# Optimization experiments

Measured on AMD Instinct MI355X. Metric: run time of the kernel, lower is better.

The kernel has to match this reference:

```python
import jax, jax.numpy as jnp
import numpy as np

N = 50000      # nodes
E = 800000     # edges
IN = 128       # in_dim
OUT = 64       # out_dim
NEG_SLOPE = 0.01  # F.leaky_relu default


def setup_inputs() -> dict:
    key = jax.random.key(0)
    k1, k2, k3, k4, k5 = jax.random.split(key, 5)
    h = jax.random.normal(k1, (N, IN), dtype=jnp.float32)
    # xavier-normal-ish scale for the two linear layers
    W_fc = jax.random.normal(k2, (OUT, IN), dtype=jnp.float32) * (2.0 / (IN + OUT)) ** 0.5
    W_attn = jax.random.normal(k3, (2 * OUT,), dtype=jnp.float32) * (2.0 / (2 * OUT + 1)) ** 0.5
    src = jax.random.randint(k4, (E,), 0, N)
    dst = jax.random.randint(k5, (E,), 0, N)
    return {"h": h, "W_fc": W_fc, "W_attn": W_attn, "src": src, "dst": dst}


def reference(h, W_fc, W_attn, src, dst):
    # z = fc(h): [N, OUT]
    z = jnp.einsum("ni,oi->no", h, W_fc)
    d = z.shape[-1]
    # per-edge attention logit: attn_fc(cat([z_src, z_dst])) == z_src@a_l + z_dst@a_r
    a_l, a_r = W_attn[:d], W_attn[d:]
    zs = z[src]                                   # [E, OUT] gather
    e = jax.nn.leaky_relu(zs @ a_l + z[dst] @ a_r, negative_slope=NEG_SLOPE)  # [E]
    # segment softmax over incoming edges of each dst node
    m = jax.ops.segment_max(e, dst, num_segments=N)          # [N]
    ex = jnp.exp(e - m[dst])                                  # [E]
    denom = jax.ops.segment_sum(ex, dst, num_segments=N)      # [N]
    alpha = ex / denom[dst]                                    # [E]
    # weighted scatter-sum of source features
    out = jax.ops.segment_sum(alpha[:, None] * zs, dst, num_segments=N)  # [N, OUT]
    return out
```

## Files before the change

### kernel.cpp

```cpp
#include <hip/hip_runtime.h>
#include <hip/hip_bf16.h>
#include <math.h>

#define IN_DIM 128
#define OUT_DIM 64
#define NEG_SLOPE 0.01f
#define BCAP 1536
#define EPT 32

typedef __attribute__((ext_vector_type(8))) short bf8_t;
typedef __attribute__((ext_vector_type(4))) float f4_t;

__device__ __forceinline__ bf8_t pack8(float4 a, float4 b) {
    union { bf8_t v; __hip_bfloat162 h[4]; } u;
    u.h[0] = __float22bfloat162_rn(make_float2(a.x, a.y));
    u.h[1] = __float22bfloat162_rn(make_float2(a.z, a.w));
    u.h[2] = __float22bfloat162_rn(make_float2(b.x, b.y));
    u.h[3] = __float22bfloat162_rn(make_float2(b.z, b.w));
    return u.v;
}

__global__ __launch_bounds__(256) void k_front(
    const int* __restrict__ src, const int* __restrict__ dst,
    int* __restrict__ bucket_cursor, unsigned* __restrict__ tmp, int E,
    const float4* __restrict__ h4, const float4* __restrict__ W4,
    const float* __restrict__ Wattn,
    __hip_bfloat16* __restrict__ zb, float* __restrict__ s_l, float* __restrict__ s_r,
    int N, int NP1)
{
    __shared__ int cntA[1024];
    __shared__ int gbase[1024];

    const int t = threadIdx.x;

    if (blockIdx.x < NP1) {
        const int base_e = blockIdx.x * (256 * EPT);

        for (int b = t; b < 1024; b += 256) cntA[b] = 0;
        __syncthreads();

        unsigned pArr[EPT];
        unsigned short rArr[EPT];
        #pragma unroll
        for (int i = 0; i < EPT; i++) {
            int ei = base_e + i * 256 + t;
            if (ei < E) {
                int s = src[ei], d = dst[ei];
                int b = d >> 6;
                pArr[i] = ((unsigned)b << 22) | ((unsigned)s << 6) | (unsigned)(d & 63);
                rArr[i] = (unsigned short)atomicAdd(&cntA[b], 1);
            } else {
                pArr[i] = 0xFFFFFFFFu;
            }
        }
        __syncthreads();

        for (int b = t; b < 1024; b += 256)
            if (cntA[b] > 0)
                gbase[b] = atomicAdd(&bucket_cursor[b], cntA[b]);
        __syncthreads();

        #pragma unroll
        for (int i = 0; i < EPT; i++) {
            unsigned p = pArr[i];
            if (p == 0xFFFFFFFFu) continue;
            int b = p >> 22;
            int slot = gbase[b] + rArr[i];
            if (slot < BCAP)
                tmp[(size_t)b * BCAP + slot] = p;
        }
    } else {
        const int lane = t & 63;
        const int wv   = t >> 6;
        const int col  = lane & 15, quad = lane >> 4;
        const int n0   = (blockIdx.x - NP1) * 64 + wv * 16;
        if (n0 >= N) return;

        bf8_t bf[4][4];
        #pragma unroll
        for (int ns = 0; ns < 4; ns++) {
            const float4* wrow = W4 + (size_t)(ns * 16 + col) * (IN_DIM / 4);
            #pragma unroll
            for (int kb = 0; kb < 4; kb++) {
                float4 x = wrow[kb * 8 + quad * 2];
                float4 y = wrow[kb * 8 + quad * 2 + 1];
                bf[kb][ns] = pack8(x, y);
            }
        }

        const int  na = n0 + col;
        const bool nv = (na < N);
        const float4* hrow = h4 + (size_t)(nv ? na : 0) * (IN_DIM / 4);
        const float4 zero = make_float4(0.f, 0.f, 0.f, 0.f);

        f4_t acc[4];
        #pragma unroll
        for (int ns = 0; ns < 4; ns++) acc[ns] = (f4_t){0.f, 0.f, 0.f, 0.f};

        #pragma unroll
        for (int kb = 0; kb < 4; kb++) {
            float4 x = nv ? hrow[kb * 8 + quad * 2]     : zero;
            float4 y = nv ? hrow[kb * 8 + quad * 2 + 1] : zero;
            bf8_t a = pack8(x, y);
            #pragma unroll
            for (int ns = 0; ns < 4; ns++)
                acc[ns] = __builtin_amdgcn_mfma_f32_16x16x32_bf16(a, bf[kb][ns], acc[ns], 0, 0, 0);
        }

        float alv[4], arv[4];
        #pragma unroll
        for (int ns = 0; ns < 4; ns++) {
            alv[ns] = Wattn[ns * 16 + col];
            arv[ns] = Wattn[OUT_DIM + ns * 16 + col];
        }
        #pragma unroll
        for (int r = 0; r < 4; r++) {
            const int nn = n0 + quad * 4 + r;
            float pl = acc[0][r] * alv[0] + acc[1][r] * alv[1] + acc[2][r] * alv[2] + acc[3][r] * alv[3];
            float pr = acc[0][r] * arv[0] + acc[1][r] * arv[1] + acc[2][r] * arv[2] + acc[3][r] * arv[3];
            #pragma unroll
            for (int o = 1; o < 16; o <<= 1) {
                pl += __shfl_xor(pl, o, 64);
                pr += __shfl_xor(pr, o, 64);
            }
            if (nn < N) {
                __hip_bfloat16* zr = zb + (size_t)nn * OUT_DIM;
                #pragma unroll
                for (int ns = 0; ns < 4; ns++)
                    zr[ns * 16 + col] = __float2bfloat16(acc[ns][r]);
                if (col == 0) { s_l[nn] = pl; s_r[nn] = pr; }
            }
        }
    }
}

__global__ __launch_bounds__(256) void k_tail(
    const unsigned* __restrict__ tmp, const int* __restrict__ bucket_cnt,
    const float* __restrict__ s_l, const float* __restrict__ s_r,
    const uint4* __restrict__ zb4, float4* __restrict__ out4, int N)
{
    __shared__ uint2 se[BCAP];
    __shared__ unsigned p2s[BCAP];
    __shared__ float exs[BCAP];
    __shared__ int cnt_s[64], off_s[64];
    __shared__ float srs[64];

    const int b = blockIdx.x, t = threadIdx.x;
    const int lane = t & 63;
    const int nbase = b * 64;
    int mb = bucket_cnt[b];
    if (mb > BCAP) mb = BCAP;

    if (t < 64) {
        cnt_s[t] = 0;
        int n = nbase + t;
        srs[t] = (n < N) ? s_r[n] : 0.f;
    }
    __syncthreads();

    const unsigned* mybuf = tmp + (size_t)b * BCAP;

    const int mb4 = mb & ~3;
    for (int i0 = t * 4; i0 < mb4; i0 += 256 * 4) {
        uint4 pv = *reinterpret_cast<const uint4*>(mybuf + i0);
        #pragma unroll
        for (int j = 0; j < 4; j++) {
            unsigned p = (j == 0) ? pv.x : (j == 1) ? pv.y : (j == 2) ? pv.z : pv.w;
            int i = i0 + j;
            int d = p & 63u;
            int s = (p >> 6) & 0xFFFFu;
            float e = s_l[s] + srs[d];
            e = (e > 0.f) ? e : NEG_SLOPE * e;
            float ex = __expf(e);
            int r = atomicAdd(&cnt_s[d], 1);
            if (r > 1023) r = 1023;
            p2s[i] = ((unsigned)r << 22) | (p & 0x3FFFFFu);
            exs[i] = ex;
        }
    }
    for (int i = mb4 + t; i < mb; i += 256) {
        unsigned p = mybuf[i];
        int d = p & 63u;
        int s = (p >> 6) & 0xFFFFu;
        float e = s_l[s] + srs[d];
        e = (e > 0.f) ? e : NEG_SLOPE * e;
        float ex = __expf(e);
        int r = atomicAdd(&cnt_s[d], 1);
        if (r > 1023) r = 1023;
        p2s[i] = ((unsigned)r << 22) | (p & 0x3FFFFFu);
        exs[i] = ex;
    }
    __syncthreads();

    if (t < 64) {
        int c = cnt_s[t];
        int inc = c;
        #pragma unroll
        for (int o = 1; o < 64; o <<= 1) {
            int v = __shfl_up(inc, o, 64);
            if (lane >= o) inc += v;
        }
        off_s[t] = inc - c;
    }
    __syncthreads();

    for (int i = t; i < mb; i += 256) {
        unsigned q = p2s[i];
        int d = q & 63u;
        int slot = off_s[d] + (int)(q >> 22);
        if (slot < BCAP)
            se[slot] = make_uint2((q >> 6) & 0xFFFFu, __float_as_uint(exs[i]));
    }
    __syncthreads();

    const int ch8 = t & 7;
    const int grp = t >> 3;

    for (int nl = grp; nl < 64; nl += 32) {
        const int n = nbase + nl;
        if (n >= N) continue;
        const int beg = off_s[nl];
        int end = beg + cnt_s[nl];
        if (end > BCAP) end = BCAP;
        float4* op = out4 + (size_t)n * 16 + ch8 * 2;

        if (end <= beg) {
            op[0] = make_float4(0.f, 0.f, 0.f, 0.f);
            op[1] = make_float4(0.f, 0.f, 0.f, 0.f);
            continue;
        }

        float a0 = 0.f, a1 = 0.f, a2 = 0.f, a3 = 0.f;
        float a4 = 0.f, a5 = 0.f, a6 = 0.f, a7 = 0.f;
        float dsum = 0.f;

        #pragma unroll 8
        for (int i = beg; i < end; ++i) {
            uint2 q = se[i];
            float ex = __uint_as_float(q.y);
            dsum += ex;
            uint4 zv = zb4[(size_t)q.x * 8 + ch8];
            float f0 = __uint_as_float(zv.x << 16);
            float f1 = __uint_as_float(zv.x & 0xffff0000u);
            float f2 = __uint_as_float(zv.y << 16);
            float f3 = __uint_as_float(zv.y & 0xffff0000u);
            float f4 = __uint_as_float(zv.z << 16);
            float f5 = __uint_as_float(zv.z & 0xffff0000u);
            float f6 = __uint_as_float(zv.w << 16);
            float f7 = __uint_as_float(zv.w & 0xffff0000u);
            a0 += ex * f0; a1 += ex * f1; a2 += ex * f2; a3 += ex * f3;
            a4 += ex * f4; a5 += ex * f5; a6 += ex * f6; a7 += ex * f7;
        }

        float inv = 1.f / dsum;
        op[0] = make_float4(a0 * inv, a1 * inv, a2 * inv, a3 * inv);
        op[1] = make_float4(a4 * inv, a5 * inv, a6 * inv, a7 * inv);
    }
}

extern "C" void kernel_launch(void* const* d_in, const int* in_sizes, int n_in,
                              void* d_out, int out_size, void* d_ws, size_t ws_size,
                              hipStream_t stream)
{
    const float* h     = (const float*)d_in[0];
    const float* Wfc   = (const float*)d_in[1];
    const float* Wattn = (const float*)d_in[2];
    const int*   src   = (const int*)d_in[3];
    const int*   dst   = (const int*)d_in[4];
    const int N = in_sizes[0] / IN_DIM;
    const int E = in_sizes[3];
    const int NBK = (N + 63) / 64;
    const int NP1 = (E + 256 * EPT - 1) / (256 * EPT);

    __hip_bfloat16* zb = (__hip_bfloat16*)d_ws;
    float* s_l     = (float*)(zb + (size_t)N * OUT_DIM);
    float* s_r     = s_l + N;
    int*   bcursor = (int*)(s_r + N);
    unsigned* tmp  = (unsigned*)(bcursor + 1024);

    const int nblk_g = (N + 63) / 64;

    hipMemsetAsync(bcursor, 0, 1024 * sizeof(int), stream);

    k_front<<<NP1 + nblk_g, 256, 0, stream>>>(src, dst, bcursor, tmp, E,
                                              (const float4*)h, (const float4*)Wfc, Wattn,
                                              zb, s_l, s_r, N, NP1);
    k_tail <<<NBK, 256, 0, stream>>>(tmp, bcursor, s_l, s_r,
                                     (const uint4*)zb, (float4*)d_out, N);
}
```

Before: 138.3 us.

## Locally sort edges by bucket in LDS before coalesced scatter to global buckets

The partition phase now runs 1024-thread blocks, each handling 16K edges. A block-wide prefix scan over the per-bucket counts places the edges in LDS ordered by bucket, and then writes them to the global bucket array in contiguous runs instead of scattered 4-byte stores. The GEMM half of the fused kernel is resized to 256 nodes per 1024-thread block. This adds 64KB of LDS plus extra barriers and scan work, which can lower occupancy and slow the GEMM blocks that share the launch.

```diff
diff --git a/kernel.cpp b/kernel.cpp
--- a/kernel.cpp
+++ b/kernel.cpp
@@ -6,7 +6,9 @@
 #define OUT_DIM 64
 #define NEG_SLOPE 0.01f
 #define BCAP 1536
-#define EPT 32
+#define P1_EPT 16
+#define P1_THREADS 1024
+#define P1_EDGES (P1_THREADS * P1_EPT)
 
 typedef __attribute__((ext_vector_type(8))) short bf8_t;
 typedef __attribute__((ext_vector_type(4))) float f4_t;
@@ -20,7 +22,7 @@
     return u.v;
 }
 
-__global__ __launch_bounds__(256) void k_front(
+__global__ __launch_bounds__(1024) void k_front(
     const int* __restrict__ src, const int* __restrict__ dst,
     int* __restrict__ bucket_cursor, unsigned* __restrict__ tmp, int E,
     const float4* __restrict__ h4, const float4* __restrict__ W4,
@@ -29,21 +31,24 @@
     int N, int NP1)
 {
     __shared__ int cntA[1024];
-    __shared__ int gbase[1024];
+    __shared__ int sbase[1024];
+    __shared__ int gbaseS[1024];
+    __shared__ int wsum[17];
+    __shared__ unsigned sortedE[P1_EDGES];
 
     const int t = threadIdx.x;
 
     if (blockIdx.x < NP1) {
-        const int base_e = blockIdx.x * (256 * EPT);
-
-        for (int b = t; b < 1024; b += 256) cntA[b] = 0;
-        __syncthreads();
-
-        unsigned pArr[EPT];
-        unsigned short rArr[EPT];
-        #pragma unroll
-        for (int i = 0; i < EPT; i++) {
-            int ei = base_e + i * 256 + t;
+        const int base_e = blockIdx.x * P1_EDGES;
+
+        cntA[t] = 0;
+        __syncthreads();
+
+        unsigned pArr[P1_EPT];
+        unsigned short rArr[P1_EPT];
+        #pragma unroll
+        for (int i = 0; i < P1_EPT; i++) {
+            int ei = base_e + i * P1_THREADS + t;
             if (ei < E) {
                 int s = src[ei], d = dst[ei];
                 int b = d >> 6;
@@ -55,17 +60,47 @@
         }
         __syncthreads();
 
-        for (int b = t; b < 1024; b += 256)
-            if (cntA[b] > 0)
-                gbase[b] = atomicAdd(&bucket_cursor[b], cntA[b]);
-        __syncthreads();
-
-        #pragma unroll
-        for (int i = 0; i < EPT; i++) {
+        const int c = cntA[t];
+        int gb = (c > 0) ? atomicAdd(&bucket_cursor[t], c) : 0;
+
+        const int lane = t & 63, wv = t >> 6;
+        int inc = c;
+        #pragma unroll
+        for (int o = 1; o < 64; o <<= 1) {
+            int v = __shfl_up(inc, o, 64);
+            if (lane >= o) inc += v;
+        }
+        if (lane == 63) wsum[wv] = inc;
+        __syncthreads();
+        if (t < 16) {
+            int wval = wsum[t];
+            int winc = wval;
+            #pragma unroll
+            for (int o = 1; o < 16; o <<= 1) {
+                int v = __shfl_up(winc, o, 64);
+                if (t >= o) winc += v;
+            }
+            wsum[t] = winc - wval;
+        }
+        __syncthreads();
+        sbase[t] = wsum[wv] + (inc - c);
+        __syncthreads();
+
+        #pragma unroll
+        for (int i = 0; i < P1_EPT; i++) {
             unsigned p = pArr[i];
             if (p == 0xFFFFFFFFu) continue;
             int b = p >> 22;
-            int slot = gbase[b] + rArr[i];
+            sortedE[sbase[b] + rArr[i]] = p;
+        }
+        gbaseS[t] = gb;
+        __syncthreads();
+
+        const int total = sbase[1023] + cntA[1023];
+        for (int i = t; i < total; i += P1_THREADS) {
+            unsigned p = sortedE[i];
+            int b = p >> 22;
+            int slot = gbaseS[b] + (i - sbase[b]);
             if (slot < BCAP)
                 tmp[(size_t)b * BCAP + slot] = p;
         }
@@ -73,7 +108,7 @@
         const int lane = t & 63;
         const int wv   = t >> 6;
         const int col  = lane & 15, quad = lane >> 4;
-        const int n0   = (blockIdx.x - NP1) * 64 + wv * 16;
+        const int n0   = (blockIdx.x - NP1) * 256 + wv * 16;
         if (n0 >= N) return;
 
         bf8_t bf[4][4];
@@ -270,7 +305,7 @@
     const int N = in_sizes[0] / IN_DIM;
     const int E = in_sizes[3];
     const int NBK = (N + 63) / 64;
-    const int NP1 = (E + 256 * EPT - 1) / (256 * EPT);
+    const int NP1 = (E + P1_EDGES - 1) / P1_EDGES;
 
     __hip_bfloat16* zb = (__hip_bfloat16*)d_ws;
     float* s_l     = (float*)(zb + (size_t)N * OUT_DIM);
@@ -278,11 +313,11 @@
     int*   bcursor = (int*)(s_r + N);
     unsigned* tmp  = (unsigned*)(bcursor + 1024);
 
-    const int nblk_g = (N + 63) / 64;
+    const int nblk_g = (N + 255) / 256;
 
     hipMemsetAsync(bcursor, 0, 1024 * sizeof(int), stream);
 
-    k_front<<<NP1 + nblk_g, 256, 0, stream>>>(src, dst, bcursor, tmp, E,
+    k_front<<<NP1 + nblk_g, P1_THREADS, 0, stream>>>(src, dst, bcursor, tmp, E,
                                               (const float4*)h, (const float4*)Wfc, Wattn,
                                               zb, s_l, s_r, N, NP1);
     k_tail <<<NBK, 256, 0, stream>>>(tmp, bcursor, s_l, s_r,
```

Measured after the change: 138.7 us. No clear change (+0.3%).
